# Performance work log

Hardware: AMD Instinct MI355X
Metric: run time of the kernel (lower is better)

Reference implementation:

```python
import jax, jax.numpy as jnp
import numpy as np

N = 50000       # nodes
F_IN = 128      # num_node_features
H = 8           # heads (conv1)
C = 32          # hidden_channels
NC = 40         # num_classes
E = 800000      # edges (before self-loops)
NEG_SLOPE = 0.2
EPS = 1e-16


def setup_inputs() -> dict:
    key = jax.random.key(0)
    ks = jax.random.split(key, 12)
    s = 0.05
    return {
        "x": jax.random.normal(ks[0], (N, F_IN), jnp.float32),
        "edge_index": jax.random.randint(ks[1], (2, E), 0, N, dtype=jnp.int64),
        # conv1: GATv2Conv(F_IN -> C, heads=8, concat=True)
        "W1l": jax.random.normal(ks[2], (F_IN, H * C), jnp.float32) * s,
        "W1r": jax.random.normal(ks[3], (F_IN, H * C), jnp.float32) * s,
        "att1": jax.random.normal(ks[4], (H, C), jnp.float32) * s,
        "b1": jnp.zeros((H * C,), jnp.float32),
        # conv2: GATv2Conv(H*C -> C, heads=1, concat=False)
        "W2l": jax.random.normal(ks[5], (H * C, C), jnp.float32) * s,
        "W2r": jax.random.normal(ks[6], (H * C, C), jnp.float32) * s,
        "att2": jax.random.normal(ks[7], (1, C), jnp.float32) * s,
        "b2": jnp.zeros((C,), jnp.float32),
        # output linear
        "Wout": jax.random.normal(ks[8], (C, NC), jnp.float32) * s,
        "bout": jnp.zeros((NC,), jnp.float32),
    }


def _gatv2(x, src, dst, Wl, Wr, att, bias, concat):
    """GATv2Conv (PyG semantics): e_ij = att . leaky_relu(Wl x_j + Wr x_i)."""
    n = x.shape[0]
    h, c = att.shape
    xl = (x @ Wl).reshape(n, h, c)  # source transform (lin_l)
    xr = (x @ Wr).reshape(n, h, c)  # target transform (lin_r)
    xs = xl[src]                    # [E,h,c] gathered source feats (x_j)
    xt = xr[dst]                    # [E,h,c] gathered target feats (x_i)
    e = jax.nn.leaky_relu(xs + xt, NEG_SLOPE)
    alpha = jnp.einsum('ehc,hc->eh', e, att)         # [E,h]
    # segment softmax over edges sharing a destination node
    amax = jax.ops.segment_max(alpha, dst, num_segments=n)
    alpha = jnp.exp(alpha - amax[dst])
    denom = jax.ops.segment_sum(alpha, dst, num_segments=n)
    alpha = alpha / (denom[dst] + EPS)
    out = jax.ops.segment_sum(xs * alpha[..., None], dst, num_segments=n)  # [n,h,c]
    out = out.reshape(n, h * c) if concat else out.mean(axis=1)
    return out + bias


def reference(x, edge_index, W1l, W1r, att1, b1, W2l, W2r, att2, b2, Wout, bout):
    n = x.shape[0]
    loops = jnp.arange(n, dtype=edge_index.dtype)
    src = jnp.concatenate([edge_index[0], loops])  # add self-loops (PyG default)
    dst = jnp.concatenate([edge_index[1], loops])
    h = jax.nn.elu(_gatv2(x, src, dst, W1l, W1r, att1, b1, concat=True))
    h = _gatv2(h, src, dst, W2l, W2r, att2, b2, concat=False)
    logits = h @ Wout + bout
    return jax.nn.log_softmax(logits, axis=1)
```

## Files before the change

### kernel.cpp

```cpp
#include <hip/hip_runtime.h>
#include <math.h>

#define NNODES 50000
#define FIN 128
#define H1 8
#define C1 32
#define HC1 256
#define C2 32
#define NCLS 40
#define NEDGE 800000
#define NTOT (NEDGE + NNODES)
#define NEG_SLOPE 0.2f
#define EPSF 1e-16f
#define SCAN_B 196

__device__ __forceinline__ float lrelu(float v) {
    return (v > 0.f) ? v : NEG_SLOPE * v;
}

__global__ __launch_bounds__(256) void hist_k(
    const int* __restrict__ ei, int* __restrict__ deg) {
    const int e = blockIdx.x * 256 + threadIdx.x;
    if (e >= NTOT) return;
    const int d = (e < NEDGE) ? ei[NEDGE + e] : e - NEDGE;
    atomicAdd(&deg[d], 1);
}

__global__ __launch_bounds__(256) void scanA(
    const int* __restrict__ deg, int* __restrict__ loc, int* __restrict__ bsum) {
    const int i = blockIdx.x * 256 + threadIdx.x;
    const int lane = threadIdx.x & 63, w = threadIdx.x >> 6;
    const int d = (i < NNODES) ? deg[i] : 0;
    int v = d;
#pragma unroll
    for (int off = 1; off < 64; off <<= 1) {
        const int u = __shfl_up(v, off);
        if (lane >= off) v += u;
    }
    __shared__ int wsum[4];
    if (lane == 63) wsum[w] = v;
    __syncthreads();
    int add = 0;
    for (int q = 0; q < w; q++) add += wsum[q];
    v += add;
    if (i < NNODES) loc[i] = v - d;
    if (threadIdx.x == 255) bsum[blockIdx.x] = v;
}

__global__ __launch_bounds__(256) void scanB(
    const int* __restrict__ bsum, int* __restrict__ boff) {
    const int t = threadIdx.x;
    const int lane = t & 63, w = t >> 6;
    const int d = (t < SCAN_B) ? bsum[t] : 0;
    int v = d;
#pragma unroll
    for (int off = 1; off < 64; off <<= 1) {
        const int u = __shfl_up(v, off);
        if (lane >= off) v += u;
    }
    __shared__ int wsum[4];
    if (lane == 63) wsum[w] = v;
    __syncthreads();
    int add = 0;
    for (int q = 0; q < w; q++) add += wsum[q];
    v += add;
    if (t < SCAN_B) boff[t] = v - d;
}

__global__ __launch_bounds__(256) void scanC(
    const int* __restrict__ loc, const int* __restrict__ boff,
    int* __restrict__ rowptr, int* __restrict__ rowcur) {
    const int i = blockIdx.x * 256 + threadIdx.x;
    if (i < NNODES) {
        const int v = loc[i] + boff[blockIdx.x];
        rowptr[i] = v;
        rowcur[i] = v;
    }
    if (i == 0) rowptr[NNODES] = NTOT;
}

__global__ __launch_bounds__(256) void scatter_k(
    const int* __restrict__ ei, int* __restrict__ rowcur,
    int* __restrict__ csr_src) {
    const int e = blockIdx.x * 256 + threadIdx.x;
    if (e >= NTOT) return;
    int s, d;
    if (e < NEDGE) { s = ei[e]; d = ei[NEDGE + e]; } else { s = d = e - NEDGE; }
    const int pos = atomicAdd(&rowcur[d], 1);
    csr_src[pos] = s;
}

#define LW1(a, b, kk)                                                     \
    { a[0] = W1l[(kk) * HC1 + tid];     b[0] = W1r[(kk) * HC1 + tid];     \
      a[1] = W1l[(kk + 1) * HC1 + tid]; b[1] = W1r[(kk + 1) * HC1 + tid]; \
      a[2] = W1l[(kk + 2) * HC1 + tid]; b[2] = W1r[(kk + 2) * HC1 + tid]; \
      a[3] = W1l[(kk + 3) * HC1 + tid]; b[3] = W1r[(kk + 3) * HC1 + tid]; }
#define FC1(wl, wr, kk)                                                   \
    { _Pragma("unroll") for (int r = 0; r < 32; r++) {                    \
        const float4 xv = *(const float4*)&xs[r][kk];                     \
        accL[r] += xv.x * wl[0]; accL[r] += xv.y * wl[1];                 \
        accL[r] += xv.z * wl[2]; accL[r] += xv.w * wl[3];                 \
        accR[r] += xv.x * wr[0]; accR[r] += xv.y * wr[1];                 \
        accR[r] += xv.z * wr[2]; accR[r] += xv.w * wr[3]; } }

__global__ __launch_bounds__(256) void gemm1(
    const float* __restrict__ x, const float* __restrict__ W1l,
    const float* __restrict__ W1r, float* __restrict__ xl1,
    float* __restrict__ xr1) {
    __shared__ float xs[32][FIN];
    const int r0 = blockIdx.x * 32;
    const int tid = threadIdx.x;
#pragma unroll
    for (int q = 0; q < 4; q++) {
        const int t4 = q * 256 + tid;
        int gr = r0 + (t4 >> 5);
        if (gr >= NNODES) gr = NNODES - 1;
        ((float4*)&xs[0][0])[t4] =
            *(const float4*)(x + (size_t)gr * FIN + (t4 & 31) * 4);
    }
    __syncthreads();
    float accL[32], accR[32];
#pragma unroll
    for (int r = 0; r < 32; r++) { accL[r] = 0.f; accR[r] = 0.f; }
    float wl0[4], wr0[4], wl1[4], wr1[4];
    LW1(wl0, wr0, 0)
    for (int k = 0; k < FIN - 8; k += 8) {
        LW1(wl1, wr1, k + 4)
        FC1(wl0, wr0, k)
        LW1(wl0, wr0, k + 8)
        FC1(wl1, wr1, k + 4)
    }
    LW1(wl1, wr1, FIN - 4)
    FC1(wl0, wr0, FIN - 8)
    FC1(wl1, wr1, FIN - 4)
#pragma unroll
    for (int r = 0; r < 32; r++) {
        const int row = r0 + r;
        if (row < NNODES) {
            xl1[(size_t)row * HC1 + tid] = accL[r];
            xr1[(size_t)row * HC1 + tid] = accR[r];
        }
    }
}

#define LW2(a, kk)                                                        \
    { a[0] = W[(kk) * C2 + c];     a[1] = W[(kk + 1) * C2 + c];           \
      a[2] = W[(kk + 2) * C2 + c]; a[3] = W[(kk + 3) * C2 + c]; }
#define FC2(wv, kk)                                                       \
    { _Pragma("unroll") for (int r = 0; r < 8; r++) {                     \
        const float4 xv = *(const float4*)&xs[rq * 8 + r][kk];            \
        acc[r] += xv.x * wv[0]; acc[r] += xv.y * wv[1];                   \
        acc[r] += xv.z * wv[2]; acc[r] += xv.w * wv[3]; } }

__global__ __launch_bounds__(256) void gemm2(
    const float* __restrict__ h1, const float* __restrict__ W2l,
    const float* __restrict__ W2r, float* __restrict__ xl2,
    float* __restrict__ xr2) {
    __shared__ float xs[32][HC1];
    const int r0 = blockIdx.x * 32;
    const int tid = threadIdx.x;
#pragma unroll
    for (int q = 0; q < 8; q++) {
        const int t4 = q * 256 + tid;
        int gr = r0 + (t4 >> 6);
        if (gr >= NNODES) gr = NNODES - 1;
        ((float4*)&xs[0][0])[t4] =
            *(const float4*)(h1 + (size_t)gr * HC1 + (t4 & 63) * 4);
    }
    __syncthreads();
    const int c = tid & 31;
    const int half = (tid >> 5) & 1;
    const int rq = tid >> 6;
    const float* __restrict__ W = half ? W2r : W2l;
    float acc[8];
#pragma unroll
    for (int r = 0; r < 8; r++) acc[r] = 0.f;
    float w0[4], w1[4];
    LW2(w0, 0)
    for (int k = 0; k < HC1 - 8; k += 8) {
        LW2(w1, k + 4)
        FC2(w0, k)
        LW2(w0, k + 8)
        FC2(w1, k + 4)
    }
    LW2(w1, HC1 - 4)
    FC2(w0, HC1 - 8)
    FC2(w1, HC1 - 4)
    float* __restrict__ outp = half ? xr2 : xl2;
#pragma unroll
    for (int r = 0; r < 8; r++) {
        const int row = r0 + rq * 8 + r;
        if (row < NNODES) outp[(size_t)row * C2 + c] = acc[r];
    }
}

__global__ __launch_bounds__(256) void conv1_node(
    const int* __restrict__ rowptr, const int* __restrict__ csr_src,
    const float* __restrict__ xl1, const float* __restrict__ xr1,
    const float* __restrict__ att1, const float* __restrict__ b1,
    float* __restrict__ h1) {
    const int d = blockIdx.x * 4 + (threadIdx.x >> 6);
    const int lane = threadIdx.x & 63;
    const int r0 = rowptr[d], r1 = rowptr[d + 1];
    const float4 xr = *(const float4*)(xr1 + (size_t)d * HC1 + lane * 4);
    const float4 av = *(const float4*)(att1 + lane * 4);
    float sum0 = 0.f, sum1 = 0.f, sum2 = 0.f, sum3 = 0.f;
    float4 acc0 = make_float4(0.f, 0.f, 0.f, 0.f);
    float4 acc1 = acc0, acc2 = acc0, acc3 = acc0;
    int j = r0;
    for (; j + 4 <= r1; j += 4) {
        const int s0 = csr_src[j],     s1 = csr_src[j + 1];
        const int s2 = csr_src[j + 2], s3 = csr_src[j + 3];
        const float4 xa = *(const float4*)(xl1 + (size_t)s0 * HC1 + lane * 4);
        const float4 xb = *(const float4*)(xl1 + (size_t)s1 * HC1 + lane * 4);
        const float4 xc = *(const float4*)(xl1 + (size_t)s2 * HC1 + lane * 4);
        const float4 xd = *(const float4*)(xl1 + (size_t)s3 * HC1 + lane * 4);
        float va = lrelu(xa.x + xr.x) * av.x + lrelu(xa.y + xr.y) * av.y +
                   lrelu(xa.z + xr.z) * av.z + lrelu(xa.w + xr.w) * av.w;
        float vb = lrelu(xb.x + xr.x) * av.x + lrelu(xb.y + xr.y) * av.y +
                   lrelu(xb.z + xr.z) * av.z + lrelu(xb.w + xr.w) * av.w;
        float vc = lrelu(xc.x + xr.x) * av.x + lrelu(xc.y + xr.y) * av.y +
                   lrelu(xc.z + xr.z) * av.z + lrelu(xc.w + xr.w) * av.w;
        float vd = lrelu(xd.x + xr.x) * av.x + lrelu(xd.y + xr.y) * av.y +
                   lrelu(xd.z + xr.z) * av.z + lrelu(xd.w + xr.w) * av.w;
        va += __shfl_xor(va, 1); vb += __shfl_xor(vb, 1);
        vc += __shfl_xor(vc, 1); vd += __shfl_xor(vd, 1);
        va += __shfl_xor(va, 2); vb += __shfl_xor(vb, 2);
        vc += __shfl_xor(vc, 2); vd += __shfl_xor(vd, 2);
        va += __shfl_xor(va, 4); vb += __shfl_xor(vb, 4);
        vc += __shfl_xor(vc, 4); vd += __shfl_xor(vd, 4);
        const float pa = __expf(va), pb = __expf(vb);
        const float pc = __expf(vc), pd = __expf(vd);
        sum0 += pa; sum1 += pb; sum2 += pc; sum3 += pd;
        acc0.x += pa * xa.x; acc0.y += pa * xa.y;
        acc0.z += pa * xa.z; acc0.w += pa * xa.w;
        acc1.x += pb * xb.x; acc1.y += pb * xb.y;
        acc1.z += pb * xb.z; acc1.w += pb * xb.w;
        acc2.x += pc * xc.x; acc2.y += pc * xc.y;
        acc2.z += pc * xc.z; acc2.w += pc * xc.w;
        acc3.x += pd * xd.x; acc3.y += pd * xd.y;
        acc3.z += pd * xd.z; acc3.w += pd * xd.w;
    }
    for (; j < r1; j++) {
        const int s0 = csr_src[j];
        const float4 xa = *(const float4*)(xl1 + (size_t)s0 * HC1 + lane * 4);
        float va = lrelu(xa.x + xr.x) * av.x + lrelu(xa.y + xr.y) * av.y +
                   lrelu(xa.z + xr.z) * av.z + lrelu(xa.w + xr.w) * av.w;
        va += __shfl_xor(va, 1); va += __shfl_xor(va, 2); va += __shfl_xor(va, 4);
        const float pa = __expf(va);
        sum0 += pa;
        acc0.x += pa * xa.x; acc0.y += pa * xa.y;
        acc0.z += pa * xa.z; acc0.w += pa * xa.w;
    }
    const float inv = 1.f / ((sum0 + sum1) + (sum2 + sum3) + EPSF);
    const float4 b = *(const float4*)(b1 + lane * 4);
    float4 o;
    o.x = ((acc0.x + acc1.x) + (acc2.x + acc3.x)) * inv + b.x;
    o.y = ((acc0.y + acc1.y) + (acc2.y + acc3.y)) * inv + b.y;
    o.z = ((acc0.z + acc1.z) + (acc2.z + acc3.z)) * inv + b.z;
    o.w = ((acc0.w + acc1.w) + (acc2.w + acc3.w)) * inv + b.w;
    o.x = (o.x > 0.f) ? o.x : expm1f(o.x);
    o.y = (o.y > 0.f) ? o.y : expm1f(o.y);
    o.z = (o.z > 0.f) ? o.z : expm1f(o.z);
    o.w = (o.w > 0.f) ? o.w : expm1f(o.w);
    *(float4*)(h1 + (size_t)d * HC1 + lane * 4) = o;
}

__global__ __launch_bounds__(256) void conv2_node(
    const int* __restrict__ rowptr, const int* __restrict__ csr_src,
    const float* __restrict__ xl2, const float* __restrict__ xr2,
    const float* __restrict__ att2, const float* __restrict__ b2,
    float* __restrict__ h2) {
    const int d = blockIdx.x * 32 + (threadIdx.x >> 3);
    const int l8 = threadIdx.x & 7;
    if (d >= NNODES) return;
    const int r0 = rowptr[d], r1 = rowptr[d + 1];
    const float4 xr = *(const float4*)(xr2 + (size_t)d * C2 + l8 * 4);
    const float4 av = *(const float4*)(att2 + l8 * 4);
    float sum0 = 0.f, sum1 = 0.f, sum2 = 0.f, sum3 = 0.f;
    float4 acc0 = make_float4(0.f, 0.f, 0.f, 0.f);
    float4 acc1 = acc0, acc2 = acc0, acc3 = acc0;
    int j = r0;
    for (; j + 4 <= r1; j += 4) {
        const int s0 = csr_src[j],     s1 = csr_src[j + 1];
        const int s2 = csr_src[j + 2], s3 = csr_src[j + 3];
        const float4 xa = *(const float4*)(xl2 + (size_t)s0 * C2 + l8 * 4);
        const float4 xb = *(const float4*)(xl2 + (size_t)s1 * C2 + l8 * 4);
        const float4 xc = *(const float4*)(xl2 + (size_t)s2 * C2 + l8 * 4);
        const float4 xd = *(const float4*)(xl2 + (size_t)s3 * C2 + l8 * 4);
        float va = lrelu(xa.x + xr.x) * av.x + lrelu(xa.y + xr.y) * av.y +
                   lrelu(xa.z + xr.z) * av.z + lrelu(xa.w + xr.w) * av.w;
        float vb = lrelu(xb.x + xr.x) * av.x + lrelu(xb.y + xr.y) * av.y +
                   lrelu(xb.z + xr.z) * av.z + lrelu(xb.w + xr.w) * av.w;
        float vc = lrelu(xc.x + xr.x) * av.x + lrelu(xc.y + xr.y) * av.y +
                   lrelu(xc.z + xr.z) * av.z + lrelu(xc.w + xr.w) * av.w;
        float vd = lrelu(xd.x + xr.x) * av.x + lrelu(xd.y + xr.y) * av.y +
                   lrelu(xd.z + xr.z) * av.z + lrelu(xd.w + xr.w) * av.w;
        va += __shfl_xor(va, 1); vb += __shfl_xor(vb, 1);
        vc += __shfl_xor(vc, 1); vd += __shfl_xor(vd, 1);
        va += __shfl_xor(va, 2); vb += __shfl_xor(vb, 2);
        vc += __shfl_xor(vc, 2); vd += __shfl_xor(vd, 2);
        va += __shfl_xor(va, 4); vb += __shfl_xor(vb, 4);
        vc += __shfl_xor(vc, 4); vd += __shfl_xor(vd, 4);
        const float pa = __expf(va), pb = __expf(vb);
        const float pc = __expf(vc), pd = __expf(vd);
        sum0 += pa; sum1 += pb; sum2 += pc; sum3 += pd;
        acc0.x += pa * xa.x; acc0.y += pa * xa.y;
        acc0.z += pa * xa.z; acc0.w += pa * xa.w;
        acc1.x += pb * xb.x; acc1.y += pb * xb.y;
        acc1.z += pb * xb.z; acc1.w += pb * xb.w;
        acc2.x += pc * xc.x; acc2.y += pc * xc.y;
        acc2.z += pc * xc.z; acc2.w += pc * xc.w;
        acc3.x += pd * xd.x; acc3.y += pd * xd.y;
        acc3.z += pd * xd.z; acc3.w += pd * xd.w;
    }
    for (; j < r1; j++) {
        const int s0 = csr_src[j];
        const float4 xa = *(const float4*)(xl2 + (size_t)s0 * C2 + l8 * 4);
        float va = lrelu(xa.x + xr.x) * av.x + lrelu(xa.y + xr.y) * av.y +
                   lrelu(xa.z + xr.z) * av.z + lrelu(xa.w + xr.w) * av.w;
        va += __shfl_xor(va, 1); va += __shfl_xor(va, 2); va += __shfl_xor(va, 4);
        const float pa = __expf(va);
        sum0 += pa;
        acc0.x += pa * xa.x; acc0.y += pa * xa.y;
        acc0.z += pa * xa.z; acc0.w += pa * xa.w;
    }
    const float inv = 1.f / ((sum0 + sum1) + (sum2 + sum3) + EPSF);
    const float4 b = *(const float4*)(b2 + l8 * 4);
    float4 o;
    o.x = ((acc0.x + acc1.x) + (acc2.x + acc3.x)) * inv + b.x;
    o.y = ((acc0.y + acc1.y) + (acc2.y + acc3.y)) * inv + b.y;
    o.z = ((acc0.z + acc1.z) + (acc2.z + acc3.z)) * inv + b.z;
    o.w = ((acc0.w + acc1.w) + (acc2.w + acc3.w)) * inv + b.w;
    *(float4*)(h2 + (size_t)d * C2 + l8 * 4) = o;
}

__global__ __launch_bounds__(256) void final_k(
    const float* __restrict__ h2, const float* __restrict__ Wout,
    const float* __restrict__ bout, float* __restrict__ out) {
    __shared__ float row[4][C2];
    const int w = threadIdx.x >> 6;
    const int node = blockIdx.x * 4 + w;
    const int lane = threadIdx.x & 63;
    if (node < NNODES && lane < C2)
        row[w][lane] = h2[(size_t)node * C2 + lane];
    __syncthreads();
    if (node >= NNODES) return;
    float logit = -INFINITY;
    if (lane < NCLS) {
        logit = bout[lane];
        for (int k = 0; k < C2; k++) logit += row[w][k] * Wout[k * NCLS + lane];
    }
    float mx = logit;
#pragma unroll
    for (int m = 1; m < 64; m <<= 1) mx = fmaxf(mx, __shfl_xor(mx, m));
    const float ex = (lane < NCLS) ? expf(logit - mx) : 0.f;
    float sm = ex;
#pragma unroll
    for (int m = 1; m < 64; m <<= 1) sm += __shfl_xor(sm, m);
    if (lane < NCLS) out[(size_t)node * NCLS + lane] = logit - mx - logf(sm);
}

extern "C" void kernel_launch(void* const* d_in, const int* in_sizes, int n_in,
                              void* d_out, int out_size, void* d_ws, size_t ws_size,
                              hipStream_t stream) {
    const float* x    = (const float*)d_in[0];
    const int*   ei   = (const int*)d_in[1];
    const float* W1l  = (const float*)d_in[2];
    const float* W1r  = (const float*)d_in[3];
    const float* att1 = (const float*)d_in[4];
    const float* b1   = (const float*)d_in[5];
    const float* W2l  = (const float*)d_in[6];
    const float* W2r  = (const float*)d_in[7];
    const float* att2 = (const float*)d_in[8];
    const float* b2   = (const float*)d_in[9];
    const float* Wout = (const float*)d_in[10];
    const float* bout = (const float*)d_in[11];
    float* out = (float*)d_out;

    float* base = (float*)d_ws;
    float* xl1 = base;
    float* xr1 = base + 12800000;
    float* xl2 = base + 25600000;
    float* xr2 = base + 27200000;
    int* ib      = (int*)(base + 28800000);
    int* deg     = ib;
    int* loc     = ib + 50000;
    int* bsum    = ib + 100000;
    int* boff    = ib + 100256;
    int* rowptr  = ib + 100512;
    int* rowcur  = ib + 150516;
    int* csr_src = ib + 200516;
    float* h1 = xr1;
    float* h2 = xr2;

    hipMemsetAsync(deg, 0, (size_t)NNODES * 4, stream);
    hist_k<<<(NTOT + 255) / 256, 256, 0, stream>>>(ei, deg);
    scanA<<<SCAN_B, 256, 0, stream>>>(deg, loc, bsum);
    scanB<<<1, 256, 0, stream>>>(bsum, boff);
    scanC<<<SCAN_B, 256, 0, stream>>>(loc, boff, rowptr, rowcur);
    scatter_k<<<(NTOT + 255) / 256, 256, 0, stream>>>(ei, rowcur, csr_src);

    gemm1<<<(NNODES + 31) / 32, 256, 0, stream>>>(x, W1l, W1r, xl1, xr1);
    conv1_node<<<NNODES / 4, 256, 0, stream>>>(rowptr, csr_src, xl1, xr1,
                                               att1, b1, h1);
    gemm2<<<(NNODES + 31) / 32, 256, 0, stream>>>(h1, W2l, W2r, xl2, xr2);
    conv2_node<<<(NNODES + 31) / 32, 256, 0, stream>>>(rowptr, csr_src, xl2,
                                                       xr2, att2, b2, h2);
    final_k<<<NNODES / 4, 256, 0, stream>>>(h2, Wout, bout, out);
}
```

Measured before the change: 506.2 us.

## Rewrite both dense GEMMs as register-blocked shared-memory tiled kernels

After: 473.2 us. 1.07x faster.

```diff
diff --git a/kernel.cpp b/kernel.cpp
--- a/kernel.cpp
+++ b/kernel.cpp
@@ -90,107 +90,141 @@
     csr_src[pos] = s;
 }
 
-#define LW1(a, b, kk)                                                     \
-    { a[0] = W1l[(kk) * HC1 + tid];     b[0] = W1r[(kk) * HC1 + tid];     \
-      a[1] = W1l[(kk + 1) * HC1 + tid]; b[1] = W1r[(kk + 1) * HC1 + tid]; \
-      a[2] = W1l[(kk + 2) * HC1 + tid]; b[2] = W1r[(kk + 2) * HC1 + tid]; \
-      a[3] = W1l[(kk + 3) * HC1 + tid]; b[3] = W1r[(kk + 3) * HC1 + tid]; }
-#define FC1(wl, wr, kk)                                                   \
-    { _Pragma("unroll") for (int r = 0; r < 32; r++) {                    \
-        const float4 xv = *(const float4*)&xs[r][kk];                     \
-        accL[r] += xv.x * wl[0]; accL[r] += xv.y * wl[1];                 \
-        accL[r] += xv.z * wl[2]; accL[r] += xv.w * wl[3];                 \
-        accR[r] += xv.x * wr[0]; accR[r] += xv.y * wr[1];                 \
-        accR[r] += xv.z * wr[2]; accR[r] += xv.w * wr[3]; } }
-
 __global__ __launch_bounds__(256) void gemm1(
     const float* __restrict__ x, const float* __restrict__ W1l,
     const float* __restrict__ W1r, float* __restrict__ xl1,
     float* __restrict__ xr1) {
-    __shared__ float xs[32][FIN];
-    const int r0 = blockIdx.x * 32;
+    __shared__ float As[64][36];
+    __shared__ float Bs[32][128];
     const int tid = threadIdx.x;
-#pragma unroll
-    for (int q = 0; q < 4; q++) {
-        const int t4 = q * 256 + tid;
-        int gr = r0 + (t4 >> 5);
-        if (gr >= NNODES) gr = NNODES - 1;
-        ((float4*)&xs[0][0])[t4] =
-            *(const float4*)(x + (size_t)gr * FIN + (t4 & 31) * 4);
-    }
-    __syncthreads();
-    float accL[32], accR[32];
-#pragma unroll
-    for (int r = 0; r < 32; r++) { accL[r] = 0.f; accR[r] = 0.f; }
-    float wl0[4], wr0[4], wl1[4], wr1[4];
-    LW1(wl0, wr0, 0)
-    for (int k = 0; k < FIN - 8; k += 8) {
-        LW1(wl1, wr1, k + 4)
-        FC1(wl0, wr0, k)
-        LW1(wl0, wr0, k + 8)
-        FC1(wl1, wr1, k + 4)
-    }
-    LW1(wl1, wr1, FIN - 4)
-    FC1(wl0, wr0, FIN - 8)
-    FC1(wl1, wr1, FIN - 4)
-#pragma unroll
-    for (int r = 0; r < 32; r++) {
-        const int row = r0 + r;
+    const int tx = tid & 15, ty = tid >> 4;
+    const int r0 = blockIdx.x * 64;
+    const int cb = blockIdx.y;
+    const float* __restrict__ W = (cb < 2) ? W1l : W1r;
+    const int c0 = (cb & 1) * 128;
+    float acc[4][8];
+#pragma unroll
+    for (int i = 0; i < 4; i++)
+#pragma unroll
+        for (int c = 0; c < 8; c++) acc[i][c] = 0.f;
+    for (int kt = 0; kt < FIN; kt += 32) {
+#pragma unroll
+        for (int q = 0; q < 2; q++) {
+            const int slot = q * 256 + tid;
+            const int row = slot >> 3, kq = slot & 7;
+            int gr = r0 + row;
+            if (gr >= NNODES) gr = NNODES - 1;
+            *(float4*)&As[row][kq * 4] =
+                *(const float4*)(x + (size_t)gr * FIN + kt + kq * 4);
+        }
+#pragma unroll
+        for (int q = 0; q < 4; q++) {
+            const int slot = q * 256 + tid;
+            const int k = slot >> 5, c4 = slot & 31;
+            *(float4*)&Bs[k][c4 * 4] =
+                *(const float4*)(W + (size_t)(kt + k) * HC1 + c0 + c4 * 4);
+        }
+        __syncthreads();
+#pragma unroll
+        for (int kk = 0; kk < 32; kk += 4) {
+#pragma unroll
+            for (int g = 0; g < 2; g++) {
+                float4 b[4];
+#pragma unroll
+                for (int k = 0; k < 4; k++)
+                    b[k] = *(const float4*)&Bs[kk + k][tx * 8 + g * 4];
+#pragma unroll
+                for (int i = 0; i < 4; i++) {
+                    const float4 a = *(const float4*)&As[ty * 4 + i][kk];
+                    acc[i][g*4+0] += a.x * b[0].x; acc[i][g*4+1] += a.x * b[0].y;
+                    acc[i][g*4+2] += a.x * b[0].z; acc[i][g*4+3] += a.x * b[0].w;
+                    acc[i][g*4+0] += a.y * b[1].x; acc[i][g*4+1] += a.y * b[1].y;
+                    acc[i][g*4+2] += a.y * b[1].z; acc[i][g*4+3] += a.y * b[1].w;
+                    acc[i][g*4+0] += a.z * b[2].x; acc[i][g*4+1] += a.z * b[2].y;
+                    acc[i][g*4+2] += a.z * b[2].z; acc[i][g*4+3] += a.z * b[2].w;
+                    acc[i][g*4+0] += a.w * b[3].x; acc[i][g*4+1] += a.w * b[3].y;
+                    acc[i][g*4+2] += a.w * b[3].z; acc[i][g*4+3] += a.w * b[3].w;
+                }
+            }
+        }
+        __syncthreads();
+    }
+    float* __restrict__ outp = (cb < 2) ? xl1 : xr1;
+    const int oc = (cb & 1) * 128 + tx * 8;
+#pragma unroll
+    for (int i = 0; i < 4; i++) {
+        const int row = r0 + ty * 4 + i;
         if (row < NNODES) {
-            xl1[(size_t)row * HC1 + tid] = accL[r];
-            xr1[(size_t)row * HC1 + tid] = accR[r];
-        }
-    }
-}
-
-#define LW2(a, kk)                                                        \
-    { a[0] = W[(kk) * C2 + c];     a[1] = W[(kk + 1) * C2 + c];           \
-      a[2] = W[(kk + 2) * C2 + c]; a[3] = W[(kk + 3) * C2 + c]; }
-#define FC2(wv, kk)                                                       \
-    { _Pragma("unroll") for (int r = 0; r < 8; r++) {                     \
-        const float4 xv = *(const float4*)&xs[rq * 8 + r][kk];            \
-        acc[r] += xv.x * wv[0]; acc[r] += xv.y * wv[1];                   \
-        acc[r] += xv.z * wv[2]; acc[r] += xv.w * wv[3]; } }
+            *(float4*)(outp + (size_t)row * HC1 + oc) =
+                make_float4(acc[i][0], acc[i][1], acc[i][2], acc[i][3]);
+            *(float4*)(outp + (size_t)row * HC1 + oc + 4) =
+                make_float4(acc[i][4], acc[i][5], acc[i][6], acc[i][7]);
+        }
+    }
+}
 
 __global__ __launch_bounds__(256) void gemm2(
     const float* __restrict__ h1, const float* __restrict__ W2l,
     const float* __restrict__ W2r, float* __restrict__ xl2,
     float* __restrict__ xr2) {
-    __shared__ float xs[32][HC1];
-    const int r0 = blockIdx.x * 32;
+    __shared__ float As[64][36];
+    __shared__ float Bs[32][64];
     const int tid = threadIdx.x;
-#pragma unroll
-    for (int q = 0; q < 8; q++) {
-        const int t4 = q * 256 + tid;
-        int gr = r0 + (t4 >> 6);
-        if (gr >= NNODES) gr = NNODES - 1;
-        ((float4*)&xs[0][0])[t4] =
-            *(const float4*)(h1 + (size_t)gr * HC1 + (t4 & 63) * 4);
-    }
-    __syncthreads();
-    const int c = tid & 31;
-    const int half = (tid >> 5) & 1;
-    const int rq = tid >> 6;
-    const float* __restrict__ W = half ? W2r : W2l;
-    float acc[8];
-#pragma unroll
-    for (int r = 0; r < 8; r++) acc[r] = 0.f;
-    float w0[4], w1[4];
-    LW2(w0, 0)
-    for (int k = 0; k < HC1 - 8; k += 8) {
-        LW2(w1, k + 4)
-        FC2(w0, k)
-        LW2(w0, k + 8)
-        FC2(w1, k + 4)
-    }
-    LW2(w1, HC1 - 4)
-    FC2(w0, HC1 - 8)
-    FC2(w1, HC1 - 4)
-    float* __restrict__ outp = half ? xr2 : xl2;
-#pragma unroll
-    for (int r = 0; r < 8; r++) {
-        const int row = r0 + rq * 8 + r;
-        if (row < NNODES) outp[(size_t)row * C2 + c] = acc[r];
+    const int tx = tid & 15, ty = tid >> 4;
+    const int r0 = blockIdx.x * 64;
+    float acc[4][4];
+#pragma unroll
+    for (int i = 0; i < 4; i++)
+#pragma unroll
+        for (int c = 0; c < 4; c++) acc[i][c] = 0.f;
+    for (int kt = 0; kt < HC1; kt += 32) {
+#pragma unroll
+        for (int q = 0; q < 2; q++) {
+            const int slot = q * 256 + tid;
+            const int row = slot >> 3, kq = slot & 7;
+            int gr = r0 + row;
+            if (gr >= NNODES) gr = NNODES - 1;
+            *(float4*)&As[row][kq * 4] =
+                *(const float4*)(h1 + (size_t)gr * HC1 + kt + kq * 4);
+        }
+#pragma unroll
+        for (int q = 0; q < 2; q++) {
+            const int slot = q * 256 + tid;
+            const int k = slot >> 4, c4 = slot & 15;
+            const float* __restrict__ Wp = (c4 < 8) ? W2l : W2r;
+            *(float4*)&Bs[k][c4 * 4] =
+                *(const float4*)(Wp + (size_t)(kt + k) * C2 + (c4 & 7) * 4);
+        }
+        __syncthreads();
+#pragma unroll
+        for (int kk = 0; kk < 32; kk += 4) {
+            float4 b[4];
+#pragma unroll
+            for (int k = 0; k < 4; k++)
+                b[k] = *(const float4*)&Bs[kk + k][tx * 4];
+#pragma unroll
+            for (int i = 0; i < 4; i++) {
+                const float4 a = *(const float4*)&As[ty * 4 + i][kk];
+                acc[i][0] += a.x * b[0].x; acc[i][1] += a.x * b[0].y;
+                acc[i][2] += a.x * b[0].z; acc[i][3] += a.x * b[0].w;
+                acc[i][0] += a.y * b[1].x; acc[i][1] += a.y * b[1].y;
+                acc[i][2] += a.y * b[1].z; acc[i][3] += a.y * b[1].w;
+                acc[i][0] += a.z * b[2].x; acc[i][1] += a.z * b[2].y;
+                acc[i][2] += a.z * b[2].z; acc[i][3] += a.z * b[2].w;
+                acc[i][0] += a.w * b[3].x; acc[i][1] += a.w * b[3].y;
+                acc[i][2] += a.w * b[3].z; acc[i][3] += a.w * b[3].w;
+            }
+        }
+        __syncthreads();
+    }
+    float* __restrict__ outp = (tx < 8) ? xl2 : xr2;
+    const int oc = (tx & 7) * 4;
+#pragma unroll
+    for (int i = 0; i < 4; i++) {
+        const int row = r0 + ty * 4 + i;
+        if (row < NNODES)
+            *(float4*)(outp + (size_t)row * C2 + oc) =
+                make_float4(acc[i][0], acc[i][1], acc[i][2], acc[i][3]);
     }
 }
 
@@ -401,10 +435,11 @@
     scanC<<<SCAN_B, 256, 0, stream>>>(loc, boff, rowptr, rowcur);
     scatter_k<<<(NTOT + 255) / 256, 256, 0, stream>>>(ei, rowcur, csr_src);
 
-    gemm1<<<(NNODES + 31) / 32, 256, 0, stream>>>(x, W1l, W1r, xl1, xr1);
+    dim3 g1((NNODES + 63) / 64, 4);
+    gemm1<<<g1, 256, 0, stream>>>(x, W1l, W1r, xl1, xr1);
     conv1_node<<<NNODES / 4, 256, 0, stream>>>(rowptr, csr_src, xl1, xr1,
                                                att1, b1, h1);
-    gemm2<<<(NNODES + 31) / 32, 256, 0, stream>>>(h1, W2l, W2r, xl2, xr2);
+    gemm2<<<(NNODES + 63) / 64, 256, 0, stream>>>(h1, W2l, W2r, xl2, xr2);
     conv2_node<<<(NNODES + 31) / 32, 256, 0, stream>>>(rowptr, csr_src, xl2,
                                                        xr2, att2, b2, h2);
     final_k<<<NNODES / 4, 256, 0, stream>>>(h2, Wout, bout, out);
```
